# Kernel tuning notes

Measured on AMD Instinct MI355X. Metric: run time of the kernel, lower is better.

## Reference

```python
import jax, jax.numpy as jnp
import numpy as np

BN_EPS = 1e-5

def conv3d(x, w, b):
    # standard 3D conv, stride 1, pad 1, NCDHW
    out = jax.lax.conv_general_dilated(x, w, (1, 1, 1), ((1, 1), (1, 1), (1, 1)),
                                       dimension_numbers=('NCDHW', 'OIDHW', 'NCDHW'))
    return out + b[None, :, None, None, None]

def batchnorm(x, gamma, beta):
    # training-mode BN over (B, D, H, W) per channel
    mu = x.mean(axis=(0, 2, 3, 4), keepdims=True)
    var = x.var(axis=(0, 2, 3, 4), keepdims=True)
    g = gamma[None, :, None, None, None]
    b = beta[None, :, None, None, None]
    return g * (x - mu) * jax.lax.rsqrt(var + BN_EPS) + b

def deform_conv3d(x, offset, weight, cpg):
    # x: [B,C,D,H,W]; offset: [B, G*27*3, D,H,W] with layout [B,G,27,(d,h,w),D,H,W]
    # weight: [C_out, C_in, 3,3,3]; kernel 3, stride 1, pad 1 -> same spatial size
    B, C, D, H, W = x.shape
    G = C // cpg
    off = offset.reshape(B, G, 27, 3, D, H, W)
    k = jnp.arange(27)
    kd = (k // 9 - 1).astype(x.dtype).reshape(1, 1, 27, 1, 1, 1)
    kh = ((k // 3) % 3 - 1).astype(x.dtype).reshape(1, 1, 27, 1, 1, 1)
    kw = (k % 3 - 1).astype(x.dtype).reshape(1, 1, 27, 1, 1, 1)
    gd = jnp.arange(D, dtype=x.dtype).reshape(1, 1, 1, D, 1, 1)
    gh = jnp.arange(H, dtype=x.dtype).reshape(1, 1, 1, 1, H, 1)
    gw = jnp.arange(W, dtype=x.dtype).reshape(1, 1, 1, 1, 1, W)
    # fractional sampling positions per (batch, group, tap, voxel): [B,G,27,D,H,W]
    pd = gd + kd + off[:, :, :, 0]
    ph = gh + kh + off[:, :, :, 1]
    pw = gw + kw + off[:, :, :, 2]
    d0 = jnp.floor(pd); h0 = jnp.floor(ph); w0 = jnp.floor(pw)
    fd = pd - d0; fh = ph - h0; fw = pw - w0
    d0i = d0.astype(jnp.int32); h0i = h0.astype(jnp.int32); w0i = w0.astype(jnp.int32)
    xg = x.reshape(B, G, cpg, D * H * W)
    N = 27 * D * H * W
    acc = jnp.zeros((B, G, cpg, 27, D, H, W), x.dtype)
    for dd in (0, 1):
        for hh in (0, 1):
            for ww in (0, 1):
                di = d0i + dd; hi = h0i + hh; wi = w0i + ww
                wgt = ((fd if dd else 1.0 - fd) * (fh if hh else 1.0 - fh)
                       * (fw if ww else 1.0 - fw))
                valid = ((di >= 0) & (di < D) & (hi >= 0) & (hi < H)
                         & (wi >= 0) & (wi < W))  # zero padding outside
                dic = jnp.clip(di, 0, D - 1)
                hic = jnp.clip(hi, 0, H - 1)
                wic = jnp.clip(wi, 0, W - 1)
                idx = ((dic * H + hic) * W + wic).reshape(B, G, 1, N)
                vals = jnp.take_along_axis(xg, jnp.broadcast_to(idx, (B, G, cpg, N)), axis=3)
                vals = vals.reshape(B, G, cpg, 27, D, H, W)
                acc = acc + (wgt * valid)[:, :, None] * vals
    wr = weight.reshape(weight.shape[0], G, cpg, 27)
    return jnp.einsum('bgckdhw,ogck->bodhw', acc, wr)

def setup_inputs() -> dict:
    key = jax.random.key(0)
    ks = jax.random.split(key, 8)
    B, C, D, H, W = 2, 64, 8, 32, 32
    cpg = 8
    Coff = (C // cpg) * 3 * 27  # 648
    fan = 1.0 / np.sqrt(C * 27)
    x = jax.random.normal(ks[0], (B, C, D, H, W), jnp.float32)
    w_off1 = jax.random.normal(ks[1], (Coff, C, 3, 3, 3), jnp.float32) * 0.01
    b_off1 = jnp.zeros((Coff,), jnp.float32)
    w1 = jax.random.normal(ks[2], (C, C, 3, 3, 3), jnp.float32) * fan
    g1 = jnp.ones((C,), jnp.float32)
    be1 = jnp.zeros((C,), jnp.float32)
    w_off2 = jax.random.normal(ks[3], (Coff, C, 3, 3, 3), jnp.float32) * 0.01
    b_off2 = jnp.zeros((Coff,), jnp.float32)
    w2 = jax.random.normal(ks[4], (C, C, 3, 3, 3), jnp.float32) * fan
    g2 = jnp.ones((C,), jnp.float32)
    be2 = jnp.zeros((C,), jnp.float32)
    return {'x': x, 'w_off1': w_off1, 'b_off1': b_off1, 'w1': w1, 'g1': g1,
            'be1': be1, 'w_off2': w_off2, 'b_off2': b_off2, 'w2': w2,
            'g2': g2, 'be2': be2, 'cpg': cpg}

def reference(x, w_off1, b_off1, w1, g1, be1, w_off2, b_off2, w2, g2, be2, cpg):
    off1 = conv3d(x, w_off1, b_off1)
    out = deform_conv3d(x, off1, w1, cpg)
    out = jax.nn.relu(batchnorm(out, g1, be1))
    off2 = conv3d(x, w_off2, b_off2)  # note: offsets computed from x, as in source
    out = deform_conv3d(out, off2, w2, cpg)
    out = batchnorm(out, g2, be2) + x
    out = jax.nn.relu(out)
    return (out, off1, off2)
```

## Files before the change

kernel.cpp:

```cpp
#include <hip/hip_runtime.h>
#include <stdint.h>

typedef unsigned short u16;
typedef __attribute__((ext_vector_type(8))) short bf16x8;
typedef __attribute__((ext_vector_type(4))) float f32x4;

#define DEV static __device__ __forceinline__

#define BB    2
#define CC    64
#define DDD   8
#define HHH   32
#define WWW   32
#define DHW   8192
#define MTOT  16384
#define GG    8
#define KTOT  1728
#define NOFF  1296
#define NOFFP 1408
#define COFF  648

#define OFF1_ELEM (BB*CC*DHW)
#define OFF2_ELEM (OFF1_ELEM + BB*COFF*DHW)

#define XCL_OFF   0ull
#define YCL_OFF   2097152ull
#define WOFF_OFF  4194304ull
#define W1_OFF    9060352ull
#define W2_OFF    9281536ull
#define C1_OFF    9502720ull
#define C2_OFF    13697024ull
#define ST1_OFF   17891328ull
#define ST2_OFF   17891840ull
#define ZPG_OFF   17892352ull
#define PART_OFF  17892608ull
#define PART2_OFF 18416896ull
#define XCL2_OFF  18449664ull
#define YCL2_OFF  20546816ull

DEV float bf2f(u16 u){ union { uint32_t i; float f; } v; v.i = ((uint32_t)u) << 16; return v.f; }
DEV u16 f2bf(float f){ union { float f; uint32_t i; } v; v.f = f;
  uint32_t r = v.i + 0x7fffu + ((v.i >> 16) & 1u); return (u16)(r >> 16); }

DEV void gld16(const void* g, void* l){
  __builtin_amdgcn_global_load_lds((const __attribute__((address_space(1))) void*)g,
                                   (__attribute__((address_space(3))) void*)l, 16, 0, 0);
}

#define PRE0 (BB*CC*DHW)
#define PRE1 (PRE0 + NOFFP*KTOT)
#define PRE2 (PRE1 + CC*KTOT)
#define PRE3 (PRE2 + CC*KTOT)
#define PRETOT (PRE3 + 128)

__global__ void k_prep(const float* __restrict__ x,
                       const float* __restrict__ wo1, const float* __restrict__ wo2,
                       const float* __restrict__ w1, const float* __restrict__ w2,
                       u16* __restrict__ xcl, u16* __restrict__ xcl2,
                       u16* __restrict__ woff,
                       u16* __restrict__ w1b, u16* __restrict__ w2b,
                       u16* __restrict__ zpg)
{
  int idx = blockIdx.x * 256 + threadIdx.x;
  if (idx < PRE0) {
    int p = idx & (DHW - 1);
    int c = (idx >> 13) & 63;
    int b = idx >> 19;
    u16 v = f2bf(x[idx]);
    xcl[(size_t)(b * DHW + p) * CC + c] = v;
    int g = c >> 3, cc = c & 7;
    xcl2[(((size_t)(b * GG + g)) * DHW + p) * 8 + cc] = v;
  } else if (idx < PRE1) {
    int j = idx - PRE0;
    int k = j % KTOT, n = j / KTOT;
    int tap = k >> 6, cin = k & 63;
    float v = 0.f;
    if (n < NOFF) {
      const float* w = (n < COFF) ? wo1 : wo2;
      int nn = (n < COFF) ? n : n - COFF;
      v = w[(size_t)nn * KTOT + cin * 27 + tap];
    }
    woff[j] = f2bf(v);
  } else if (idx < PRE2) {
    int j = idx - PRE1;
    int k = j % KTOT, n = j / KTOT;
    int tap = k >> 6, cin = k & 63;
    w1b[j] = f2bf(w1[(size_t)n * KTOT + cin * 27 + tap]);
  } else if (idx < PRE3) {
    int j = idx - PRE2;
    int k = j % KTOT, n = j / KTOT;
    int tap = k >> 6, cin = k & 63;
    w2b[j] = f2bf(w2[(size_t)n * KTOT + cin * 27 + tap]);
  } else if (idx < PRETOT) {
    zpg[idx - PRE3] = 0;
  }
}

__global__ __launch_bounds__(256) void k_gemm_off(
    const u16* __restrict__ xcl, const u16* __restrict__ woff,
    const float* __restrict__ boff1, const float* __restrict__ boff2,
    float* __restrict__ dout, const u16* __restrict__ zpg)
{
  __shared__ u16 Al[128 * 64];
  __shared__ u16 Bl[128 * 64];
  const int tid = threadIdx.x;
  const int wv = tid >> 6, lane = tid & 63;
  const int m0 = blockIdx.x * 128;
  const int n0 = blockIdx.y * 128;
  const int lr = lane >> 3, lc = lane & 7;
  const int lcs = (lc ^ lr) << 3;
  const int b  = m0 >> 13;
  const int p0 = m0 & (DHW - 1);
  int ad[4], ah[4], aw[4];
  #pragma unroll
  for (int i = 0; i < 4; ++i) {
    int p = p0 + wv * 32 + i * 8 + lr;
    ad[i] = p >> 10; ah[i] = (p >> 5) & 31; aw[i] = p & 31;
  }
  const size_t xb = (size_t)b * DHW * CC;

  f32x4 acc[4][4] = {};
  const int wm = wv >> 1, wn = wv & 1;
  const int r16 = lane & 15, q = lane >> 4;
  const int rs = r16 & 7;

  for (int t = 0; t < 27; ++t) {
    int kd = t / 9 - 1, kh = (t / 3) % 3 - 1, kw = t % 3 - 1;
    #pragma unroll
    for (int i = 0; i < 4; ++i) {
      int d2 = ad[i] + kd, h2 = ah[i] + kh, w2 = aw[i] + kw;
      bool ok = ((unsigned)d2 < DDD) & ((unsigned)h2 < HHH) & ((unsigned)w2 < WWW);
      const u16* src = ok ? (xcl + xb + (size_t)((d2 << 10) + (h2 << 5) + w2) * CC + lcs)
                          : zpg;
      gld16(src, &Al[(wv * 32 + i * 8) * 64]);
    }
    #pragma unroll
    for (int i = 0; i < 4; ++i) {
      int r = wv * 32 + i * 8 + lr;
      const u16* src = woff + (size_t)(n0 + r) * KTOT + t * 64 + lcs;
      gld16(src, &Bl[(wv * 32 + i * 8) * 64]);
    }
    __syncthreads();
    #pragma unroll
    for (int kk = 0; kk < 2; ++kk) {
      const int cs = ((kk * 4 + q) ^ rs) << 3;
      bf16x8 af[4], bfr[4];
      #pragma unroll
      for (int i = 0; i < 4; ++i)
        af[i] = *(const bf16x8*)&Al[(wm * 64 + i * 16 + r16) * 64 + cs];
      #pragma unroll
      for (int j = 0; j < 4; ++j)
        bfr[j] = *(const bf16x8*)&Bl[(wn * 64 + j * 16 + r16) * 64 + cs];
      #pragma unroll
      for (int i = 0; i < 4; ++i)
        #pragma unroll
        for (int j = 0; j < 4; ++j)
          acc[i][j] = __builtin_amdgcn_mfma_f32_16x16x32_bf16(af[i], bfr[j], acc[i][j], 0, 0, 0);
    }
    __syncthreads();
  }

  float biasj[4]; int ncj[4];
  #pragma unroll
  for (int j = 0; j < 4; ++j) {
    int nc = n0 + wn * 64 + j * 16 + r16;
    ncj[j] = nc;
    biasj[j] = (nc < NOFF) ? ((nc < COFF) ? boff1[nc] : boff2[nc - COFF]) : 0.f;
  }
  #pragma unroll
  for (int i = 0; i < 4; ++i) {
    int mrow = m0 + wm * 64 + i * 16 + q * 4;
    int bb = mrow >> 13, p = mrow & (DHW - 1);
    #pragma unroll
    for (int j = 0; j < 4; ++j) {
      int nc = ncj[j];
      if (nc < NOFF) {
        int ch = (nc < COFF) ? nc : nc - COFF;
        size_t base = (nc < COFF) ? (size_t)OFF1_ELEM : (size_t)OFF2_ELEM;
        f32x4 v = acc[i][j] + biasj[j];
        *(f32x4*)(dout + base + ((size_t)(bb * COFF + ch)) * DHW + p) = v;
      }
    }
  }
}

__global__ __launch_bounds__(256) void k_deform(
    const u16* __restrict__ src2, const float* __restrict__ offs,
    const u16* __restrict__ wB, float* __restrict__ cdst,
    const u16* __restrict__ zpg, float* __restrict__ part)
{
  __shared__ u16 Al[2 * 16 * 64];
  __shared__ u16 Bl[2 * 64 * 64];
  const int tid = threadIdx.x;
  const int wv = tid >> 6, lane = tid & 63;
  const int mrow0 = blockIdx.x * 16;
  const int b  = mrow0 >> 13;
  const int p0 = mrow0 & (DHW - 1);

  const int th = wv >> 1;
  const int pl = (lane & 7) + 8 * (wv & 1);
  const int g  = lane >> 3;
  const int p  = p0 + pl;
  const int d = p >> 10, h = (p >> 5) & 31, w = p & 31;
  const u16* sb = src2 + (((size_t)(b * GG + g)) * DHW) * 8;
  const size_t obase = ((size_t)(b * COFF + g * 81)) * DHW + p;
  u16* awp = &Al[th * 1024 + pl * 64 + ((g ^ (pl & 7)) << 3)];

  const int lr = lane >> 3, lc = lane & 7;
  const int lcs = (lc ^ lr) << 3;

  f32x4 acc = {};
  const int r16 = lane & 15, q = lane >> 4;
  const int rs = r16 & 7;

  for (int ph = 0; ph < 14; ++ph) {
    #pragma unroll
    for (int i = 0; i < 4; ++i) {
      int tb = 2 * ph + (i >> 1);
      int row = (i & 1) * 32 + wv * 8 + lr;
      const u16* s = (tb < 27) ? (wB + (size_t)row * KTOT + tb * 64 + lcs) : zpg;
      gld16(s, &Bl[(i >> 1) * 4096 + (((i & 1) * 32 + wv * 8) * 64)]);
    }
    {
      int t = 2 * ph + th;
      float a8[8] = {0.f,0.f,0.f,0.f,0.f,0.f,0.f,0.f};
      if (t < 27) {
        int kd = t / 9 - 1, kh = (t / 3) % 3 - 1, kw = t % 3 - 1;
        size_t ob = obase + (size_t)(t * 3) * DHW;
        float pd = (float)(d + kd) + offs[ob];
        float phh = (float)(h + kh) + offs[ob + DHW];
        float pw = (float)(w + kw) + offs[ob + 2 * DHW];
        float fd0 = floorf(pd), fh0 = floorf(phh), fw0 = floorf(pw);
        float fd = pd - fd0, fh = phh - fh0, fw = pw - fw0;
        int d0 = (int)fd0, h0 = (int)fh0, w0 = (int)fw0;
        #pragma unroll
        for (int dd = 0; dd < 2; ++dd) {
          float wd = dd ? fd : 1.f - fd;
          int di = d0 + dd;
          #pragma unroll
          for (int hh = 0; hh < 2; ++hh) {
            float wh = hh ? fh : 1.f - fh;
            int hi = h0 + hh;
            const u16* rowb = sb + (size_t)((di << 10) + (hi << 5)) * 8;
            #pragma unroll
            for (int ww = 0; ww < 2; ++ww) {
              int wi = w0 + ww;
              if (((unsigned)di < DDD) && ((unsigned)hi < HHH) && ((unsigned)wi < WWW)) {
                float wgt = wd * wh * (ww ? fw : 1.f - fw);
                bf16x8 v = *(const bf16x8*)(rowb + (size_t)wi * 8);
                #pragma unroll
                for (int c = 0; c < 8; ++c) a8[c] += wgt * bf2f((u16)v[c]);
              }
            }
          }
        }
      }
      union { bf16x8 v; u16 u[8]; } o;
      #pragma unroll
      for (int c = 0; c < 8; ++c) o.u[c] = f2bf(a8[c]);
      *(bf16x8*)awp = o.v;
    }
    __syncthreads();
    #pragma unroll
    for (int tt = 0; tt < 2; ++tt) {
      #pragma unroll
      for (int kk = 0; kk < 2; ++kk) {
        const int cs = ((kk * 4 + q) ^ rs) << 3;
        bf16x8 af = *(const bf16x8*)&Al[tt * 1024 + r16 * 64 + cs];
        bf16x8 bf_ = *(const bf16x8*)&Bl[tt * 4096 + (wv * 16 + r16) * 64 + cs];
        acc = __builtin_amdgcn_mfma_f32_16x16x32_bf16(af, bf_, acc, 0, 0, 0);
      }
    }
    __syncthreads();
  }

  {
    int nc = wv * 16 + r16;
    int mr = mrow0 + q * 4;
    #pragma unroll
    for (int r = 0; r < 4; ++r)
      cdst[(size_t)(mr + r) * CC + nc] = acc[r];
  }

  {
    float s  = acc[0] + acc[1] + acc[2] + acc[3];
    float s2 = acc[0]*acc[0] + acc[1]*acc[1] + acc[2]*acc[2] + acc[3]*acc[3];
    s  += __shfl_down(s, 16, 64);  s  += __shfl_down(s, 32, 64);
    s2 += __shfl_down(s2, 16, 64); s2 += __shfl_down(s2, 32, 64);
    if (lane < 16) {
      part[(size_t)blockIdx.x * 128 + wv * 16 + lane] = s;
      part[(size_t)blockIdx.x * 128 + 64 + wv * 16 + lane] = s2;
    }
  }
}

__global__ void k_bnred(const float* __restrict__ part, float* __restrict__ part2)
{
  int k = blockIdx.x, tid = threadIdx.x;
  float s = 0.f;
  #pragma unroll
  for (int j = 0; j < 16; ++j)
    s += part[(size_t)(k * 16 + j) * 128 + tid];
  part2[(size_t)k * 128 + tid] = s;
}

__global__ void k_bnfin(const float* __restrict__ part2, const float* __restrict__ gamma,
                        const float* __restrict__ beta, float* __restrict__ stats)
{
  int tid = threadIdx.x;
  float S = 0.f;
  #pragma unroll 8
  for (int k = 0; k < 64; ++k) S += part2[(size_t)k * 128 + tid];
  __shared__ float sh[128];
  sh[tid] = S;
  __syncthreads();
  if (tid < 64) {
    float mu = sh[tid] / (float)MTOT;
    float var = sh[64 + tid] / (float)MTOT - mu * mu;
    float sc = gamma[tid] / sqrtf(var + 1e-5f);
    stats[tid] = sc;
    stats[64 + tid] = beta[tid] - mu * sc;
  }
}

__global__ void k_apply1(const float* __restrict__ c1, const float* __restrict__ st,
                         u16* __restrict__ ycl2)
{
  int idx = blockIdx.x * 256 + threadIdx.x;
  int g = idx & 7;
  int p = (idx >> 3) & (DHW - 1);
  int b = idx >> 16;
  const float* row = c1 + (size_t)(b * DHW + p) * CC + g * 8;
  union { bf16x8 v; u16 u[8]; } o;
  #pragma unroll
  for (int c = 0; c < 8; ++c) {
    int ch = g * 8 + c;
    float v = st[ch] * row[c] + st[64 + ch];
    o.u[c] = f2bf(fmaxf(v, 0.f));
  }
  *(bf16x8*)(ycl2 + ((((size_t)(b * GG + g)) * DHW + p) * 8)) = o.v;
}

__global__ void k_apply2(const float* __restrict__ c2, const float* __restrict__ st,
                         const float* __restrict__ x, float* __restrict__ out)
{
  int idx = blockIdx.x * 256 + threadIdx.x;
  if (idx >= BB * CC * DHW) return;
  int p = idx & (DHW - 1);
  int n = (idx >> 13) & 63;
  int b = idx >> 19;
  float v = st[n] * c2[(size_t)(b * DHW + p) * CC + n] + st[64 + n] + x[idx];
  out[idx] = fmaxf(v, 0.f);
}

extern "C" void kernel_launch(void* const* d_in, const int* in_sizes, int n_in,
                              void* d_out, int out_size, void* d_ws, size_t ws_size,
                              hipStream_t stream)
{
  (void)in_sizes; (void)n_in; (void)out_size; (void)ws_size;
  const float* x      = (const float*)d_in[0];
  const float* w_off1 = (const float*)d_in[1];
  const float* b_off1 = (const float*)d_in[2];
  const float* w1     = (const float*)d_in[3];
  const float* g1     = (const float*)d_in[4];
  const float* be1    = (const float*)d_in[5];
  const float* w_off2 = (const float*)d_in[6];
  const float* b_off2 = (const float*)d_in[7];
  const float* w2     = (const float*)d_in[8];
  const float* g2     = (const float*)d_in[9];
  const float* be2    = (const float*)d_in[10];

  char* ws = (char*)d_ws;
  u16*   xcl   = (u16*)(ws + XCL_OFF);
  u16*   xcl2  = (u16*)(ws + XCL2_OFF);
  u16*   ycl2  = (u16*)(ws + YCL2_OFF);
  u16*   woff  = (u16*)(ws + WOFF_OFF);
  u16*   w1b   = (u16*)(ws + W1_OFF);
  u16*   w2b   = (u16*)(ws + W2_OFF);
  float* c1    = (float*)(ws + C1_OFF);
  float* c2    = (float*)(ws + C2_OFF);
  float* st1   = (float*)(ws + ST1_OFF);
  float* st2   = (float*)(ws + ST2_OFF);
  u16*   zpg   = (u16*)(ws + ZPG_OFF);
  float* part  = (float*)(ws + PART_OFF);
  float* part2 = (float*)(ws + PART2_OFF);
  float* out   = (float*)d_out;

  k_prep<<<(PRETOT + 255) / 256, 256, 0, stream>>>(
      x, w_off1, w_off2, w1, w2, xcl, xcl2, woff, w1b, w2b, zpg);

  k_gemm_off<<<dim3(MTOT / 128, NOFFP / 128), 256, 0, stream>>>(
      xcl, woff, b_off1, b_off2, out, zpg);

  k_deform<<<MTOT / 16, 256, 0, stream>>>(xcl2, out + OFF1_ELEM, w1b, c1, zpg, part);
  k_bnred<<<64, 128, 0, stream>>>(part, part2);
  k_bnfin<<<1, 128, 0, stream>>>(part2, g1, be1, st1);
  k_apply1<<<(BB * DHW * GG) / 256, 256, 0, stream>>>(c1, st1, ycl2);

  k_deform<<<MTOT / 16, 256, 0, stream>>>(ycl2, out + OFF2_ELEM, w2b, c2, zpg, part);
  k_bnred<<<64, 128, 0, stream>>>(part, part2);
  k_bnfin<<<1, 128, 0, stream>>>(part2, g2, be2, st2);
  k_apply2<<<(BB*CC*DHW) / 256, 256, 0, stream>>>(c2, st2, x, out);
}
```

Measured before the change: 238.6 us.

## Double threads per block in offset GEMM and deform kernels with split-K reduction

Both the offset-conv GEMM and the deformable-conv kernel move from 256 to 512 threads per block. In the GEMM each wave now covers 32 instead of 64 rows of the 128x128 tile. In the deform kernel four taps are sampled per phase instead of two, which halves the phase loop from 14 to 7 iterations. The two wave halves then split the K dimension and combine their partial accumulators through shared memory before the output and BN partial-sum stores. The aim is more parallel gather latency hiding and fewer barrier rounds, at the cost of larger shared memory, an extra reduction step, and possibly lower occupancy.

```diff
diff --git a/kernel.cpp b/kernel.cpp
--- a/kernel.cpp
+++ b/kernel.cpp
@@ -24,7 +24,6 @@
 #define OFF2_ELEM (OFF1_ELEM + BB*COFF*DHW)
 
 #define XCL_OFF   0ull
-#define YCL_OFF   2097152ull
 #define WOFF_OFF  4194304ull
 #define W1_OFF    9060352ull
 #define W2_OFF    9281536ull
@@ -96,7 +95,7 @@
   }
 }
 
-__global__ __launch_bounds__(256) void k_gemm_off(
+__global__ __launch_bounds__(512) void k_gemm_off(
     const u16* __restrict__ xcl, const u16* __restrict__ woff,
     const float* __restrict__ boff1, const float* __restrict__ boff2,
     float* __restrict__ dout, const u16* __restrict__ zpg)
@@ -111,15 +110,15 @@
   const int lcs = (lc ^ lr) << 3;
   const int b  = m0 >> 13;
   const int p0 = m0 & (DHW - 1);
-  int ad[4], ah[4], aw[4];
+  int ad[2], ah[2], aw[2];
   #pragma unroll
-  for (int i = 0; i < 4; ++i) {
-    int p = p0 + wv * 32 + i * 8 + lr;
+  for (int i = 0; i < 2; ++i) {
+    int p = p0 + i * 64 + wv * 8 + lr;
     ad[i] = p >> 10; ah[i] = (p >> 5) & 31; aw[i] = p & 31;
   }
   const size_t xb = (size_t)b * DHW * CC;
 
-  f32x4 acc[4][4] = {};
+  f32x4 acc[2][4] = {};
   const int wm = wv >> 1, wn = wv & 1;
   const int r16 = lane & 15, q = lane >> 4;
   const int rs = r16 & 7;
@@ -127,32 +126,32 @@
   for (int t = 0; t < 27; ++t) {
     int kd = t / 9 - 1, kh = (t / 3) % 3 - 1, kw = t % 3 - 1;
     #pragma unroll
-    for (int i = 0; i < 4; ++i) {
+    for (int i = 0; i < 2; ++i) {
       int d2 = ad[i] + kd, h2 = ah[i] + kh, w2 = aw[i] + kw;
       bool ok = ((unsigned)d2 < DDD) & ((unsigned)h2 < HHH) & ((unsigned)w2 < WWW);
       const u16* src = ok ? (xcl + xb + (size_t)((d2 << 10) + (h2 << 5) + w2) * CC + lcs)
                           : zpg;
-      gld16(src, &Al[(wv * 32 + i * 8) * 64]);
-    }
-    #pragma unroll
-    for (int i = 0; i < 4; ++i) {
-      int r = wv * 32 + i * 8 + lr;
-      const u16* src = woff + (size_t)(n0 + r) * KTOT + t * 64 + lcs;
-      gld16(src, &Bl[(wv * 32 + i * 8) * 64]);
+      gld16(src, &Al[(i * 64 + wv * 8) * 64]);
+    }
+    #pragma unroll
+    for (int i = 0; i < 2; ++i) {
+      int r = n0 + i * 64 + wv * 8 + lr;
+      const u16* src = woff + (size_t)r * KTOT + t * 64 + lcs;
+      gld16(src, &Bl[(i * 64 + wv * 8) * 64]);
     }
     __syncthreads();
     #pragma unroll
     for (int kk = 0; kk < 2; ++kk) {
       const int cs = ((kk * 4 + q) ^ rs) << 3;
-      bf16x8 af[4], bfr[4];
+      bf16x8 af[2], bfr[4];
       #pragma unroll
-      for (int i = 0; i < 4; ++i)
-        af[i] = *(const bf16x8*)&Al[(wm * 64 + i * 16 + r16) * 64 + cs];
+      for (int i = 0; i < 2; ++i)
+        af[i] = *(const bf16x8*)&Al[(wm * 32 + i * 16 + r16) * 64 + cs];
       #pragma unroll
       for (int j = 0; j < 4; ++j)
         bfr[j] = *(const bf16x8*)&Bl[(wn * 64 + j * 16 + r16) * 64 + cs];
       #pragma unroll
-      for (int i = 0; i < 4; ++i)
+      for (int i = 0; i < 2; ++i)
         #pragma unroll
         for (int j = 0; j < 4; ++j)
           acc[i][j] = __builtin_amdgcn_mfma_f32_16x16x32_bf16(af[i], bfr[j], acc[i][j], 0, 0, 0);
@@ -168,8 +167,8 @@
     biasj[j] = (nc < NOFF) ? ((nc < COFF) ? boff1[nc] : boff2[nc - COFF]) : 0.f;
   }
   #pragma unroll
-  for (int i = 0; i < 4; ++i) {
-    int mrow = m0 + wm * 64 + i * 16 + q * 4;
+  for (int i = 0; i < 2; ++i) {
+    int mrow = m0 + wm * 32 + i * 16 + q * 4;
     int bb = mrow >> 13, p = mrow & (DHW - 1);
     #pragma unroll
     for (int j = 0; j < 4; ++j) {
@@ -184,51 +183,54 @@
   }
 }
 
-__global__ __launch_bounds__(256) void k_deform(
+__global__ __launch_bounds__(512) void k_deform(
     const u16* __restrict__ src2, const float* __restrict__ offs,
     const u16* __restrict__ wB, float* __restrict__ cdst,
     const u16* __restrict__ zpg, float* __restrict__ part)
 {
-  __shared__ u16 Al[2 * 16 * 64];
-  __shared__ u16 Bl[2 * 64 * 64];
+  __shared__ u16 Al[4 * 16 * 64];
+  __shared__ u16 Bl[4 * 64 * 64];
   const int tid = threadIdx.x;
   const int wv = tid >> 6, lane = tid & 63;
   const int mrow0 = blockIdx.x * 16;
   const int b  = mrow0 >> 13;
   const int p0 = mrow0 & (DHW - 1);
 
-  const int th = wv >> 1;
-  const int pl = (lane & 7) + 8 * (wv & 1);
+  const int tq = tid >> 7;
+  const int pl = (lane & 7) + 8 * ((tid >> 6) & 1);
   const int g  = lane >> 3;
   const int p  = p0 + pl;
   const int d = p >> 10, h = (p >> 5) & 31, w = p & 31;
   const u16* sb = src2 + (((size_t)(b * GG + g)) * DHW) * 8;
   const size_t obase = ((size_t)(b * COFF + g * 81)) * DHW + p;
-  u16* awp = &Al[th * 1024 + pl * 64 + ((g ^ (pl & 7)) << 3)];
-
-  const int lr = lane >> 3, lc = lane & 7;
-  const int lcs = (lc ^ lr) << 3;
+  u16* awp = &Al[tq * 1024 + pl * 64 + ((g ^ (pl & 7)) << 3)];
 
   f32x4 acc = {};
   const int r16 = lane & 15, q = lane >> 4;
   const int rs = r16 & 7;
-
-  for (int ph = 0; ph < 14; ++ph) {
+  const int oc = wv & 3;
+  const int kh = wv >> 2;
+
+  for (int ph = 0; ph < 7; ++ph) {
     #pragma unroll
     for (int i = 0; i < 4; ++i) {
-      int tb = 2 * ph + (i >> 1);
-      int row = (i & 1) * 32 + wv * 8 + lr;
-      const u16* s = (tb < 27) ? (wB + (size_t)row * KTOT + tb * 64 + lcs) : zpg;
-      gld16(s, &Bl[(i >> 1) * 4096 + (((i & 1) * 32 + wv * 8) * 64)]);
+      int ci = wv * 256 + i * 64 + lane;
+      int tq2 = ci >> 9;
+      int row = (ci >> 3) & 63;
+      int c   = ci & 7;
+      int tb  = 4 * ph + tq2;
+      const u16* s = (tb < 27) ? (wB + (size_t)row * KTOT + tb * 64 + ((c ^ (row & 7)) << 3))
+                               : zpg;
+      gld16(s, &Bl[(size_t)(wv * 256 + i * 64) * 8]);
     }
     {
-      int t = 2 * ph + th;
+      int t = 4 * ph + tq;
       float a8[8] = {0.f,0.f,0.f,0.f,0.f,0.f,0.f,0.f};
       if (t < 27) {
-        int kd = t / 9 - 1, kh = (t / 3) % 3 - 1, kw = t % 3 - 1;
+        int kd = t / 9 - 1, khh = (t / 3) % 3 - 1, kw = t % 3 - 1;
         size_t ob = obase + (size_t)(t * 3) * DHW;
         float pd = (float)(d + kd) + offs[ob];
-        float phh = (float)(h + kh) + offs[ob + DHW];
+        float phh = (float)(h + khh) + offs[ob + DHW];
         float pw = (float)(w + kw) + offs[ob + 2 * DHW];
         float fd0 = floorf(pd), fh0 = floorf(phh), fw0 = floorf(pw);
         float fd = pd - fd0, fh = phh - fh0, fw = pw - fw0;
@@ -262,34 +264,42 @@
     }
     __syncthreads();
     #pragma unroll
-    for (int tt = 0; tt < 2; ++tt) {
+    for (int tt2 = 0; tt2 < 2; ++tt2) {
+      const int tt = kh * 2 + tt2;
       #pragma unroll
       for (int kk = 0; kk < 2; ++kk) {
         const int cs = ((kk * 4 + q) ^ rs) << 3;
         bf16x8 af = *(const bf16x8*)&Al[tt * 1024 + r16 * 64 + cs];
-        bf16x8 bf_ = *(const bf16x8*)&Bl[tt * 4096 + (wv * 16 + r16) * 64 + cs];
+        bf16x8 bf_ = *(const bf16x8*)&Bl[tt * 4096 + (oc * 16 + r16) * 64 + cs];
         acc = __builtin_amdgcn_mfma_f32_16x16x32_bf16(af, bf_, acc, 0, 0, 0);
       }
     }
     __syncthreads();
   }
 
-  {
-    int nc = wv * 16 + r16;
+  float* fs = (float*)Al;
+  if (kh == 1) {
+    #pragma unroll
+    for (int r = 0; r < 4; ++r) fs[oc * 256 + lane * 4 + r] = acc[r];
+  }
+  __syncthreads();
+  if (kh == 0) {
+    #pragma unroll
+    for (int r = 0; r < 4; ++r) acc[r] += fs[oc * 256 + lane * 4 + r];
+
+    int nc = oc * 16 + r16;
     int mr = mrow0 + q * 4;
     #pragma unroll
     for (int r = 0; r < 4; ++r)
       cdst[(size_t)(mr + r) * CC + nc] = acc[r];
-  }
-
-  {
+
     float s  = acc[0] + acc[1] + acc[2] + acc[3];
     float s2 = acc[0]*acc[0] + acc[1]*acc[1] + acc[2]*acc[2] + acc[3]*acc[3];
     s  += __shfl_down(s, 16, 64);  s  += __shfl_down(s, 32, 64);
     s2 += __shfl_down(s2, 16, 64); s2 += __shfl_down(s2, 32, 64);
     if (lane < 16) {
-      part[(size_t)blockIdx.x * 128 + wv * 16 + lane] = s;
-      part[(size_t)blockIdx.x * 128 + 64 + wv * 16 + lane] = s2;
+      part[(size_t)blockIdx.x * 128 + oc * 16 + lane] = s;
+      part[(size_t)blockIdx.x * 128 + 64 + oc * 16 + lane] = s2;
     }
   }
 }
@@ -389,15 +399,15 @@
   k_prep<<<(PRETOT + 255) / 256, 256, 0, stream>>>(
       x, w_off1, w_off2, w1, w2, xcl, xcl2, woff, w1b, w2b, zpg);
 
-  k_gemm_off<<<dim3(MTOT / 128, NOFFP / 128), 256, 0, stream>>>(
+  k_gemm_off<<<dim3(MTOT / 128, NOFFP / 128), 512, 0, stream>>>(
       xcl, woff, b_off1, b_off2, out, zpg);
 
-  k_deform<<<MTOT / 16, 256, 0, stream>>>(xcl2, out + OFF1_ELEM, w1b, c1, zpg, part);
+  k_deform<<<MTOT / 16, 512, 0, stream>>>(xcl2, out + OFF1_ELEM, w1b, c1, zpg, part);
   k_bnred<<<64, 128, 0, stream>>>(part, part2);
   k_bnfin<<<1, 128, 0, stream>>>(part2, g1, be1, st1);
   k_apply1<<<(BB * DHW * GG) / 256, 256, 0, stream>>>(c1, st1, ycl2);
 
-  k_deform<<<MTOT / 16, 256, 0, stream>>>(ycl2, out + OFF2_ELEM, w2b, c2, zpg, part);
+  k_deform<<<MTOT / 16, 512, 0, stream>>>(ycl2, out + OFF2_ELEM, w2b, c2, zpg, part);
   k_bnred<<<64, 128, 0, stream>>>(part, part2);
   k_bnfin<<<1, 128, 0, stream>>>(part2, g2, be2, st2);
   k_apply2<<<(BB*CC*DHW) / 256, 256, 0, stream>>>(c2, st2, x, out);
```

New measurement: 242.6 us. No clear change (+1.7%).
